# Kernel tuning notes

Measured on AMD Instinct MI355X. Metric: run time of the kernel, lower is better.

## Reference

```python
import jax, jax.numpy as jnp
import numpy as np

EPS = 1e-6

def setup_inputs() -> dict:
    key = jax.random.key(0)
    ks = jax.random.split(key, 8)
    B, C, H, W = 8, 256, 128, 128
    d = C // 8  # scale=8
    return {
        "x": jax.random.normal(ks[0], (B, C, H, W), dtype=jnp.float32),
        "wq": jax.random.normal(ks[1], (d, C), dtype=jnp.float32) * 0.05,
        "bq": jax.random.normal(ks[2], (d,), dtype=jnp.float32) * 0.05,
        "wk": jax.random.normal(ks[3], (d, C), dtype=jnp.float32) * 0.05,
        "bk": jax.random.normal(ks[4], (d,), dtype=jnp.float32) * 0.05,
        "wv": jax.random.normal(ks[5], (C, C), dtype=jnp.float32) * 0.05,
        "bv": jax.random.normal(ks[6], (C,), dtype=jnp.float32) * 0.05,
        "gamma": jax.random.normal(ks[7], (1,), dtype=jnp.float32) * 0.05,
    }

def reference(x, wq, bq, wk, bk, wv, bv, gamma):
    B, C, H, W = x.shape
    N = H * W
    xf = x.reshape(B, C, N)  # flatten spatial
    # 1x1 convs == channel-mixing matmuls
    Q = jax.nn.softplus(jnp.einsum('dc,bcn->bnd', wq, xf) + bq[None, None, :])  # [B,N,d]
    K = jax.nn.softplus(jnp.einsum('dc,bcn->bdn', wk, xf) + bk[None, :, None])  # [B,d,N]
    V = jnp.einsum('ec,bcn->ben', wv, xf) + bv[None, :, None]                    # [B,C,N]
    KV = jnp.einsum('bmn,bcn->bmc', K, V)                # [B,d,C]
    norm = 1.0 / jnp.einsum('bnm,bm->bn', Q, K.sum(-1) + EPS)  # [B,N]
    wv_out = jnp.einsum('bnm,bmc,bn->bcn', Q, KV, norm)  # [B,C,N]
    return x + gamma * wv_out.reshape(B, C, H, W)
```

## Files before the change

kernel.cpp:

```cpp
#include <hip/hip_runtime.h>

#define NB 8
#define NC 256
#define ND 32
#define NN 16384
#define EPSF 1e-6f

__device__ __forceinline__ float softplusf(float v) {
    return fmaxf(v, 0.0f) + log1pf(__expf(-fabsf(v)));
}

__global__ __launch_bounds__(256) void kA(
    const float* __restrict__ x, const float* __restrict__ wk,
    const float* __restrict__ bk, float* __restrict__ part,
    float* __restrict__ kxf, float* __restrict__ ksum, int use_part)
{
    __shared__ __align__(16) float xsT[32 * 258];
    __shared__ __align__(16) float wkM[32 * 260];
    __shared__ __align__(16) float Ks [32 * 36];

    const int t    = threadIdx.x;
    const int b    = blockIdx.x >> 6;
    const int tile = blockIdx.x & 63;
    const int n0   = tile << 8;
    const float* xb = x + (size_t)b * NC * NN;

    #pragma unroll
    for (int i = 0; i < 32; ++i) {
        int f = t + (i << 8);
        wkM[(f >> 8) * 260 + (f & 255)] = wk[f];
    }

    const int jA  = t & 31;
    const int m0A = (t >> 5) << 2;
    const int m0X = (t >> 6) << 3;
    const int eX  = t & 63;

    float bkr[4];
    #pragma unroll
    for (int r = 0; r < 4; ++r) bkr[r] = bk[m0A + r];

    float acc[8][4];
    #pragma unroll
    for (int a = 0; a < 8; ++a)
        #pragma unroll
        for (int kk = 0; kk < 4; ++kk) acc[a][kk] = 0.0f;
    float ksacc[4] = {0.f, 0.f, 0.f, 0.f};

    for (int st = 0; st < 8; ++st) {
        const int n1 = n0 + (st << 5);
        __syncthreads();
        #pragma unroll
        for (int i = 0; i < 32; ++i) {
            int f = t + (i << 8);
            int c = f >> 5, j = f & 31;
            xsT[j * 258 + c] = xb[c * NN + n1 + j];
        }
        __syncthreads();

        float kacc[4] = {0.f, 0.f, 0.f, 0.f};
        #pragma unroll 4
        for (int c = 0; c < 256; c += 4) {
            float2 xa = *(const float2*)&xsT[jA * 258 + c];
            float2 xc = *(const float2*)&xsT[jA * 258 + c + 2];
            #pragma unroll
            for (int r = 0; r < 4; ++r) {
                float4 w = *(const float4*)&wkM[(m0A + r) * 260 + c];
                kacc[r] = fmaf(xa.x, w.x, kacc[r]);
                kacc[r] = fmaf(xa.y, w.y, kacc[r]);
                kacc[r] = fmaf(xc.x, w.z, kacc[r]);
                kacc[r] = fmaf(xc.y, w.w, kacc[r]);
            }
        }
        #pragma unroll
        for (int r = 0; r < 4; ++r) {
            float kv_ = softplusf(kacc[r] + bkr[r]);
            Ks[jA * 36 + m0A + r] = kv_;
            ksacc[r] += kv_;
        }
        __syncthreads();

        #pragma unroll 2
        for (int j = 0; j < 32; ++j) {
            const float* kp = &Ks[j * 36 + m0X];
            float4 ka = *(const float4*)kp;
            float4 kb = *(const float4*)(kp + 4);
            const float km[8] = {ka.x, ka.y, ka.z, ka.w, kb.x, kb.y, kb.z, kb.w};
            float xv[4];
            #pragma unroll
            for (int kk = 0; kk < 4; ++kk) xv[kk] = xsT[j * 258 + eX + (kk << 6)];
            #pragma unroll
            for (int a = 0; a < 8; ++a)
                #pragma unroll
                for (int kk = 0; kk < 4; ++kk)
                    acc[a][kk] = fmaf(km[a], xv[kk], acc[a][kk]);
        }
    }

    #pragma unroll
    for (int r = 0; r < 4; ++r) {
        float v = ksacc[r];
        for (int o = 16; o; o >>= 1) v += __shfl_down(v, o, 32);
        if (jA == 0) atomicAdd(&ksum[b * 32 + m0A + r], v);
    }

    if (use_part) {
        float* dst = part + (size_t)blockIdx.x * 8192;
        #pragma unroll
        for (int a = 0; a < 8; ++a)
            #pragma unroll
            for (int kk = 0; kk < 4; ++kk)
                dst[(m0X + a) * 256 + eX + (kk << 6)] = acc[a][kk];
    } else {
        float* dst = kxf + (size_t)b * 8192;
        #pragma unroll
        for (int a = 0; a < 8; ++a)
            #pragma unroll
            for (int kk = 0; kk < 4; ++kk)
                atomicAdd(&dst[(m0X + a) * 256 + eX + (kk << 6)], acc[a][kk]);
    }
}

__global__ __launch_bounds__(256) void kR(const float* __restrict__ part,
                                          float* __restrict__ kxf)
{
    int idx = blockIdx.x * 256 + threadIdx.x;
    int b = idx >> 13, f = idx & 8191;
    float s = 0.f;
    #pragma unroll 8
    for (int tl = 0; tl < 64; ++tl)
        s += part[(size_t)(b * 64 + tl) * 8192 + f];
    kxf[idx] = s;
}

__global__ __launch_bounds__(256) void kB(
    const float* __restrict__ kxf, const float* __restrict__ ksum,
    const float* __restrict__ wv, const float* __restrict__ bv,
    float* __restrict__ kv)
{
    __shared__ float wvT[256 * 33];
    __shared__ float kxs[32 * 257];

    const int t  = threadIdx.x;
    const int b  = blockIdx.x >> 3;
    const int c0 = (blockIdx.x & 7) << 5;

    #pragma unroll
    for (int i = 0; i < 32; ++i) {
        int f = t + (i << 8);
        int r = f >> 8, e = f & 255;
        wvT[e * 33 + r]  = wv[(size_t)(c0 + r) * 256 + e];
        kxs[r * 257 + e] = kxf[b * 8192 + f];
    }
    __syncthreads();

    const int cl = t & 31, mq = t >> 5;
    float a0 = 0.f, a1 = 0.f, a2 = 0.f, a3 = 0.f;
    for (int e = 0; e < 256; ++e) {
        float wvv = wvT[e * 33 + cl];
        a0 = fmaf(kxs[(mq     ) * 257 + e], wvv, a0);
        a1 = fmaf(kxs[(mq +  8) * 257 + e], wvv, a1);
        a2 = fmaf(kxs[(mq + 16) * 257 + e], wvv, a2);
        a3 = fmaf(kxs[(mq + 24) * 257 + e], wvv, a3);
    }
    const int c = c0 + cl;
    const float bvc = bv[c];
    const float* ks = ksum + b * 32;
    float* kvb = kv + (size_t)b * 8192;
    kvb[(mq     ) * 256 + c] = a0 + bvc * ks[mq     ];
    kvb[(mq +  8) * 256 + c] = a1 + bvc * ks[mq +  8];
    kvb[(mq + 16) * 256 + c] = a2 + bvc * ks[mq + 16];
    kvb[(mq + 24) * 256 + c] = a3 + bvc * ks[mq + 24];
}

__global__ __launch_bounds__(512) void kC(
    const float* __restrict__ x, const float* __restrict__ wq,
    const float* __restrict__ bq, const float* __restrict__ kv,
    const float* __restrict__ ksum, const float* __restrict__ gamma,
    float* __restrict__ out)
{
    __shared__ __align__(16) float xs [256 * 64];
    __shared__ __align__(16) float wqM[32 * 260];
    __shared__ __align__(16) float Qs [32 * 68];
    __shared__ __align__(16) float KVs[32 * 256];
    __shared__ float ksE[32];

    const int t    = threadIdx.x;
    const int b    = blockIdx.x >> 6;
    const int tile = blockIdx.x & 63;
    const int n0   = tile << 8;
    const float* xb = x + (size_t)b * NC * NN;
    const float g = gamma[0];

    #pragma unroll
    for (int i = 0; i < 16; ++i) {
        int f = t + (i << 9);
        wqM[(f >> 8) * 260 + (f & 255)] = wq[f];
        KVs[f] = kv[(size_t)b * 8192 + f];
    }
    if (t < 32) ksE[t] = ksum[b * 32 + t] + EPSF;

    const int jsQ = t & 15;
    const int mQ  = t >> 4;
    const float bqm = bq[mQ];
    const int jO  = t & 63;
    const int c0O = (t >> 6) << 5;

    for (int st = 0; st < 4; ++st) {
        const int n1 = n0 + (st << 6);
        __syncthreads();
        #pragma unroll
        for (int i = 0; i < 32; ++i) {
            int f = t + (i << 9);
            int c = f >> 6, j = f & 63;
            xs[f] = xb[c * NN + n1 + j];
        }
        __syncthreads();

        float qa[4] = {0.f, 0.f, 0.f, 0.f};
        #pragma unroll 4
        for (int c = 0; c < 256; c += 4) {
            float4 w  = *(const float4*)&wqM[mQ * 260 + c];
            float4 x0 = *(const float4*)&xs[(c + 0) * 64 + (jsQ << 2)];
            float4 x1 = *(const float4*)&xs[(c + 1) * 64 + (jsQ << 2)];
            float4 x2 = *(const float4*)&xs[(c + 2) * 64 + (jsQ << 2)];
            float4 x3 = *(const float4*)&xs[(c + 3) * 64 + (jsQ << 2)];
            qa[0] = fmaf(w.x, x0.x, qa[0]); qa[0] = fmaf(w.y, x1.x, qa[0]);
            qa[0] = fmaf(w.z, x2.x, qa[0]); qa[0] = fmaf(w.w, x3.x, qa[0]);
            qa[1] = fmaf(w.x, x0.y, qa[1]); qa[1] = fmaf(w.y, x1.y, qa[1]);
            qa[1] = fmaf(w.z, x2.y, qa[1]); qa[1] = fmaf(w.w, x3.y, qa[1]);
            qa[2] = fmaf(w.x, x0.z, qa[2]); qa[2] = fmaf(w.y, x1.z, qa[2]);
            qa[2] = fmaf(w.z, x2.z, qa[2]); qa[2] = fmaf(w.w, x3.z, qa[2]);
            qa[3] = fmaf(w.x, x0.w, qa[3]); qa[3] = fmaf(w.y, x1.w, qa[3]);
            qa[3] = fmaf(w.z, x2.w, qa[3]); qa[3] = fmaf(w.w, x3.w, qa[3]);
        }
        #pragma unroll
        for (int r = 0; r < 4; ++r)
            Qs[mQ * 68 + (jsQ << 2) + r] = softplusf(qa[r] + bqm);
        __syncthreads();

        float q[32];
        #pragma unroll
        for (int m = 0; m < 32; ++m) q[m] = Qs[m * 68 + jO];
        float den = 0.f;
        #pragma unroll
        for (int m = 0; m < 32; ++m) den = fmaf(q[m], ksE[m], den);
        const float nrm = g / den;

        #pragma unroll
        for (int cc = 0; cc < 8; ++cc) {
            const int c = c0O + (cc << 2);
            float s0 = 0.f, s1 = 0.f, s2 = 0.f, s3 = 0.f;
            #pragma unroll
            for (int m = 0; m < 32; ++m) {
                float4 kvv = *(const float4*)&KVs[m * 256 + c];
                s0 = fmaf(q[m], kvv.x, s0);
                s1 = fmaf(q[m], kvv.y, s1);
                s2 = fmaf(q[m], kvv.z, s2);
                s3 = fmaf(q[m], kvv.w, s3);
            }
            size_t base = (size_t)b * NC * NN + (size_t)c * NN + n1 + jO;
            out[base         ] = xs[(c + 0) * 64 + jO] + nrm * s0;
            out[base +     NN] = xs[(c + 1) * 64 + jO] + nrm * s1;
            out[base + 2 * NN] = xs[(c + 2) * 64 + jO] + nrm * s2;
            out[base + 3 * NN] = xs[(c + 3) * 64 + jO] + nrm * s3;
        }
    }
}

extern "C" void kernel_launch(void* const* d_in, const int* in_sizes, int n_in,
                              void* d_out, int out_size, void* d_ws, size_t ws_size,
                              hipStream_t stream)
{
    (void)in_sizes; (void)n_in; (void)out_size;
    const float* x     = (const float*)d_in[0];
    const float* wq    = (const float*)d_in[1];
    const float* bq    = (const float*)d_in[2];
    const float* wk    = (const float*)d_in[3];
    const float* bk    = (const float*)d_in[4];
    const float* wv    = (const float*)d_in[5];
    const float* bv    = (const float*)d_in[6];
    const float* gamma = (const float*)d_in[7];
    float* out = (float*)d_out;

    char* ws = (char*)d_ws;
    float* kxf  = (float*)(ws);
    float* ksum = (float*)(ws + 262144);
    float* kv   = (float*)(ws + 263168);
    float* part = (float*)(ws + 525312);
    const size_t need_part = 525312ull + 512ull * 8192ull * 4ull;
    const int use_part = (ws_size >= need_part) ? 1 : 0;

    hipMemsetAsync(ksum, 0, 1024, stream);
    if (!use_part) hipMemsetAsync(kxf, 0, 262144, stream);

    kA<<<dim3(512), dim3(256), 0, stream>>>(x, wk, bk, part, kxf, ksum, use_part);
    if (use_part) kR<<<dim3(256), dim3(256), 0, stream>>>(part, kxf);
    kB<<<dim3(64), dim3(256), 0, stream>>>(kxf, ksum, wv, bv, kv);
    kC<<<dim3(512), dim3(512), 0, stream>>>(x, wq, bq, kv, ksum, gamma, out);
}
```

Before: 435.1 us.

## Use bf16 MFMA for K/Q projections, KX accumulation and output in kA/kC

Rewrites the channel-mixing matmuls in kA and kC to use bf16 16x16x32 MFMA instructions, with fp32 inputs converted to bf16 in registers and LDS. kC is retiled into 1024 blocks of 256 threads, and the residual x is re-read from global memory instead of staged fp32 in LDS. The aim is to replace scalar FMA loops with matrix-core throughput and to cut LDS footprint so more blocks fit per CU. The cost is bf16 rounding in Q, K, x and KV, which may reduce accuracy, plus extra global reads of x.

```diff
diff --git a/kernel.cpp b/kernel.cpp
--- a/kernel.cpp
+++ b/kernel.cpp
@@ -1,4 +1,5 @@
 #include <hip/hip_runtime.h>
+#include <hip/hip_bf16.h>
 
 #define NB 8
 #define NC 256
@@ -6,8 +7,19 @@
 #define NN 16384
 #define EPSF 1e-6f
 
+typedef __attribute__((ext_vector_type(8))) short short8;
+typedef __attribute__((ext_vector_type(4))) float float4v;
+
 __device__ __forceinline__ float softplusf(float v) {
     return fmaxf(v, 0.0f) + log1pf(__expf(-fabsf(v)));
+}
+
+__device__ __forceinline__ unsigned short f2bf(float f) {
+    __hip_bfloat16 h = __float2bfloat16(f);
+    return *reinterpret_cast<unsigned short*>(&h);
+}
+__device__ __forceinline__ unsigned int pk2bf(float lo, float hi) {
+    return (unsigned int)f2bf(lo) | ((unsigned int)f2bf(hi) << 16);
 }
 
 __global__ __launch_bounds__(256) void kA(
@@ -15,109 +27,116 @@
     const float* __restrict__ bk, float* __restrict__ part,
     float* __restrict__ kxf, float* __restrict__ ksum, int use_part)
 {
-    __shared__ __align__(16) float xsT[32 * 258];
-    __shared__ __align__(16) float wkM[32 * 260];
-    __shared__ __align__(16) float Ks [32 * 36];
-
-    const int t    = threadIdx.x;
-    const int b    = blockIdx.x >> 6;
-    const int tile = blockIdx.x & 63;
-    const int n0   = tile << 8;
+    __shared__ __align__(16) unsigned char smem[35840];
+    unsigned short* xsT = (unsigned short*)smem;
+    float*          KXs = (float*)smem;
+    unsigned short* Klt = (unsigned short*)(smem + 33280);
+
+    const int t  = threadIdx.x;
+    const int b  = blockIdx.x >> 6;
+    const int n0 = (blockIdx.x & 63) << 8;
     const float* xb = x + (size_t)b * NC * NN;
 
-    #pragma unroll
-    for (int i = 0; i < 32; ++i) {
-        int f = t + (i << 8);
-        wkM[(f >> 8) * 260 + (f & 255)] = wk[f];
-    }
-
-    const int jA  = t & 31;
-    const int m0A = (t >> 5) << 2;
-    const int m0X = (t >> 6) << 3;
-    const int eX  = t & 63;
-
+    const int w = t >> 6, l = t & 63, q = l >> 4, ln = l & 15;
+    const int mt = w & 1, ct = w >> 1;
+
+    short8 wkf[8];
+    #pragma unroll
+    for (int ks = 0; ks < 8; ++ks) {
+        const float* wp = wk + (16 * mt + ln) * 256 + 32 * ks + 8 * q;
+        float4 a = *(const float4*)wp;
+        float4 c = *(const float4*)(wp + 4);
+        short8 f;
+        f[0] = (short)f2bf(a.x); f[1] = (short)f2bf(a.y);
+        f[2] = (short)f2bf(a.z); f[3] = (short)f2bf(a.w);
+        f[4] = (short)f2bf(c.x); f[5] = (short)f2bf(c.y);
+        f[6] = (short)f2bf(c.z); f[7] = (short)f2bf(c.w);
+        wkf[ks] = f;
+    }
     float bkr[4];
     #pragma unroll
-    for (int r = 0; r < 4; ++r) bkr[r] = bk[m0A + r];
-
-    float acc[8][4];
-    #pragma unroll
-    for (int a = 0; a < 8; ++a)
-        #pragma unroll
-        for (int kk = 0; kk < 4; ++kk) acc[a][kk] = 0.0f;
-    float ksacc[4] = {0.f, 0.f, 0.f, 0.f};
-
-    for (int st = 0; st < 8; ++st) {
-        const int n1 = n0 + (st << 5);
-        __syncthreads();
-        #pragma unroll
-        for (int i = 0; i < 32; ++i) {
-            int f = t + (i << 8);
-            int c = f >> 5, j = f & 31;
-            xsT[j * 258 + c] = xb[c * NN + n1 + j];
-        }
-        __syncthreads();
-
-        float kacc[4] = {0.f, 0.f, 0.f, 0.f};
-        #pragma unroll 4
-        for (int c = 0; c < 256; c += 4) {
-            float2 xa = *(const float2*)&xsT[jA * 258 + c];
-            float2 xc = *(const float2*)&xsT[jA * 258 + c + 2];
-            #pragma unroll
-            for (int r = 0; r < 4; ++r) {
-                float4 w = *(const float4*)&wkM[(m0A + r) * 260 + c];
-                kacc[r] = fmaf(xa.x, w.x, kacc[r]);
-                kacc[r] = fmaf(xa.y, w.y, kacc[r]);
-                kacc[r] = fmaf(xc.x, w.z, kacc[r]);
-                kacc[r] = fmaf(xc.y, w.w, kacc[r]);
-            }
+    for (int r = 0; r < 4; ++r) bkr[r] = bk[16 * mt + 4 * q + r];
+
+    float ksumacc[4] = {0.f, 0.f, 0.f, 0.f};
+    float4v kxacc[4][2];
+    #pragma unroll
+    for (int i = 0; i < 4; ++i)
+        #pragma unroll
+        for (int m2 = 0; m2 < 2; ++m2) kxacc[i][m2] = (float4v){0.f, 0.f, 0.f, 0.f};
+    const float4v zf = {0.f, 0.f, 0.f, 0.f};
+
+    for (int ch = 0; ch < 8; ++ch) {
+        const int nc = n0 + (ch << 5);
+        __syncthreads();
+        #pragma unroll
+        for (int i = 0; i < 16; ++i) {
+            int p = t + (i << 8);
+            int n_ = p & 31, cp = p >> 5;
+            float v0 = xb[(size_t)(2 * cp) * NN + nc + n_];
+            float v1 = xb[(size_t)(2 * cp + 1) * NN + nc + n_];
+            *(unsigned int*)&xsT[n_ * 264 + 2 * cp] = pk2bf(v0, v1);
+        }
+        __syncthreads();
+
+        float4v kacc = zf;
+        const int ncol = 16 * ct + ln;
+        #pragma unroll
+        for (int ks = 0; ks < 8; ++ks) {
+            short8 bfr = *(const short8*)&xsT[ncol * 264 + 32 * ks + 8 * q];
+            kacc = __builtin_amdgcn_mfma_f32_16x16x32_bf16(wkf[ks], bfr, kacc, 0, 0, 0);
         }
         #pragma unroll
         for (int r = 0; r < 4; ++r) {
             float kv_ = softplusf(kacc[r] + bkr[r]);
-            Ks[jA * 36 + m0A + r] = kv_;
-            ksacc[r] += kv_;
-        }
-        __syncthreads();
-
-        #pragma unroll 2
-        for (int j = 0; j < 32; ++j) {
-            const float* kp = &Ks[j * 36 + m0X];
-            float4 ka = *(const float4*)kp;
-            float4 kb = *(const float4*)(kp + 4);
-            const float km[8] = {ka.x, ka.y, ka.z, ka.w, kb.x, kb.y, kb.z, kb.w};
-            float xv[4];
+            ksumacc[r] += kv_;
+            Klt[(16 * mt + 4 * q + r) * 40 + ncol] = f2bf(kv_);
+        }
+        __syncthreads();
+
+        #pragma unroll
+        for (int i = 0; i < 4; ++i) {
+            const int e = 16 * (4 * w + i) + ln;
+            const float* xp = xb + (size_t)e * NN + nc + 8 * q;
+            float4 xa = *(const float4*)xp;
+            float4 xc = *(const float4*)(xp + 4);
+            short8 af;
+            af[0] = (short)f2bf(xa.x); af[1] = (short)f2bf(xa.y);
+            af[2] = (short)f2bf(xa.z); af[3] = (short)f2bf(xa.w);
+            af[4] = (short)f2bf(xc.x); af[5] = (short)f2bf(xc.y);
+            af[6] = (short)f2bf(xc.z); af[7] = (short)f2bf(xc.w);
             #pragma unroll
-            for (int kk = 0; kk < 4; ++kk) xv[kk] = xsT[j * 258 + eX + (kk << 6)];
+            for (int m2 = 0; m2 < 2; ++m2) {
+                short8 bfr = *(const short8*)&Klt[(16 * m2 + ln) * 40 + 8 * q];
+                kxacc[i][m2] = __builtin_amdgcn_mfma_f32_16x16x32_bf16(af, bfr, kxacc[i][m2], 0, 0, 0);
+            }
+        }
+    }
+
+    #pragma unroll
+    for (int r = 0; r < 4; ++r) {
+        float v = ksumacc[r];
+        v += __shfl_xor(v, 1); v += __shfl_xor(v, 2);
+        v += __shfl_xor(v, 4); v += __shfl_xor(v, 8);
+        if (ln == 0) atomicAdd(&ksum[b * 32 + 16 * mt + 4 * q + r], v);
+    }
+
+    __syncthreads();
+    #pragma unroll
+    for (int i = 0; i < 4; ++i)
+        #pragma unroll
+        for (int m2 = 0; m2 < 2; ++m2)
             #pragma unroll
-            for (int a = 0; a < 8; ++a)
-                #pragma unroll
-                for (int kk = 0; kk < 4; ++kk)
-                    acc[a][kk] = fmaf(km[a], xv[kk], acc[a][kk]);
-        }
-    }
-
-    #pragma unroll
-    for (int r = 0; r < 4; ++r) {
-        float v = ksacc[r];
-        for (int o = 16; o; o >>= 1) v += __shfl_down(v, o, 32);
-        if (jA == 0) atomicAdd(&ksum[b * 32 + m0A + r], v);
-    }
-
+            for (int r = 0; r < 4; ++r)
+                KXs[(16 * m2 + ln) * 260 + 16 * (4 * w + i) + 4 * q + r] = kxacc[i][m2][r];
+    __syncthreads();
     if (use_part) {
         float* dst = part + (size_t)blockIdx.x * 8192;
         #pragma unroll
-        for (int a = 0; a < 8; ++a)
-            #pragma unroll
-            for (int kk = 0; kk < 4; ++kk)
-                dst[(m0X + a) * 256 + eX + (kk << 6)] = acc[a][kk];
+        for (int i = 0; i < 32; ++i) dst[i * 256 + t] = KXs[i * 260 + t];
     } else {
         float* dst = kxf + (size_t)b * 8192;
         #pragma unroll
-        for (int a = 0; a < 8; ++a)
-            #pragma unroll
-            for (int kk = 0; kk < 4; ++kk)
-                atomicAdd(&dst[(m0X + a) * 256 + eX + (kk << 6)], acc[a][kk]);
+        for (int i = 0; i < 32; ++i) atomicAdd(&dst[i * 256 + t], KXs[i * 260 + t]);
     }
 }
 
@@ -173,97 +192,108 @@
     kvb[(mq + 24) * 256 + c] = a3 + bvc * ks[mq + 24];
 }
 
-__global__ __launch_bounds__(512) void kC(
+__global__ __launch_bounds__(256) void kC(
     const float* __restrict__ x, const float* __restrict__ wq,
     const float* __restrict__ bq, const float* __restrict__ kv,
     const float* __restrict__ ksum, const float* __restrict__ gamma,
     float* __restrict__ out)
 {
-    __shared__ __align__(16) float xs [256 * 64];
-    __shared__ __align__(16) float wqM[32 * 260];
-    __shared__ __align__(16) float Qs [32 * 68];
-    __shared__ __align__(16) float KVs[32 * 256];
-    __shared__ float ksE[32];
-
-    const int t    = threadIdx.x;
-    const int b    = blockIdx.x >> 6;
-    const int tile = blockIdx.x & 63;
-    const int n0   = tile << 8;
+    __shared__ __align__(16) unsigned short xsT[32 * 264];
+    __shared__ __align__(16) unsigned short Qs [32 * 40];
+    __shared__ float denp[2 * 32];
+
+    const int t  = threadIdx.x;
+    const int b  = blockIdx.x >> 7;
+    const int n0 = (blockIdx.x & 127) << 5 << 2;
     const float* xb = x + (size_t)b * NC * NN;
+    float* ob = out + (size_t)b * NC * NN;
     const float g = gamma[0];
 
-    #pragma unroll
-    for (int i = 0; i < 16; ++i) {
-        int f = t + (i << 9);
-        wqM[(f >> 8) * 260 + (f & 255)] = wq[f];
-        KVs[f] = kv[(size_t)b * 8192 + f];
-    }
-    if (t < 32) ksE[t] = ksum[b * 32 + t] + EPSF;
-
-    const int jsQ = t & 15;
-    const int mQ  = t >> 4;
-    const float bqm = bq[mQ];
-    const int jO  = t & 63;
-    const int c0O = (t >> 6) << 5;
-
-    for (int st = 0; st < 4; ++st) {
-        const int n1 = n0 + (st << 6);
-        __syncthreads();
-        #pragma unroll
-        for (int i = 0; i < 32; ++i) {
-            int f = t + (i << 9);
-            int c = f >> 6, j = f & 63;
-            xs[f] = xb[c * NN + n1 + j];
-        }
-        __syncthreads();
-
-        float qa[4] = {0.f, 0.f, 0.f, 0.f};
-        #pragma unroll 4
-        for (int c = 0; c < 256; c += 4) {
-            float4 w  = *(const float4*)&wqM[mQ * 260 + c];
-            float4 x0 = *(const float4*)&xs[(c + 0) * 64 + (jsQ << 2)];
-            float4 x1 = *(const float4*)&xs[(c + 1) * 64 + (jsQ << 2)];
-            float4 x2 = *(const float4*)&xs[(c + 2) * 64 + (jsQ << 2)];
-            float4 x3 = *(const float4*)&xs[(c + 3) * 64 + (jsQ << 2)];
-            qa[0] = fmaf(w.x, x0.x, qa[0]); qa[0] = fmaf(w.y, x1.x, qa[0]);
-            qa[0] = fmaf(w.z, x2.x, qa[0]); qa[0] = fmaf(w.w, x3.x, qa[0]);
-            qa[1] = fmaf(w.x, x0.y, qa[1]); qa[1] = fmaf(w.y, x1.y, qa[1]);
-            qa[1] = fmaf(w.z, x2.y, qa[1]); qa[1] = fmaf(w.w, x3.y, qa[1]);
-            qa[2] = fmaf(w.x, x0.z, qa[2]); qa[2] = fmaf(w.y, x1.z, qa[2]);
-            qa[2] = fmaf(w.z, x2.z, qa[2]); qa[2] = fmaf(w.w, x3.z, qa[2]);
-            qa[3] = fmaf(w.x, x0.w, qa[3]); qa[3] = fmaf(w.y, x1.w, qa[3]);
-            qa[3] = fmaf(w.z, x2.w, qa[3]); qa[3] = fmaf(w.w, x3.w, qa[3]);
-        }
-        #pragma unroll
-        for (int r = 0; r < 4; ++r)
-            Qs[mQ * 68 + (jsQ << 2) + r] = softplusf(qa[r] + bqm);
-        __syncthreads();
-
-        float q[32];
-        #pragma unroll
-        for (int m = 0; m < 32; ++m) q[m] = Qs[m * 68 + jO];
-        float den = 0.f;
-        #pragma unroll
-        for (int m = 0; m < 32; ++m) den = fmaf(q[m], ksE[m], den);
-        const float nrm = g / den;
-
-        #pragma unroll
-        for (int cc = 0; cc < 8; ++cc) {
-            const int c = c0O + (cc << 2);
-            float s0 = 0.f, s1 = 0.f, s2 = 0.f, s3 = 0.f;
+    const int w = t >> 6, l = t & 63, q = l >> 4, ln = l & 15;
+    const int mt = w & 1, ct = w >> 1;
+
+    short8 wqf[8];
+    #pragma unroll
+    for (int ks = 0; ks < 8; ++ks) {
+        const float* wp = wq + (16 * mt + ln) * 256 + 32 * ks + 8 * q;
+        float4 a = *(const float4*)wp;
+        float4 c = *(const float4*)(wp + 4);
+        short8 f;
+        f[0] = (short)f2bf(a.x); f[1] = (short)f2bf(a.y);
+        f[2] = (short)f2bf(a.z); f[3] = (short)f2bf(a.w);
+        f[4] = (short)f2bf(c.x); f[5] = (short)f2bf(c.y);
+        f[6] = (short)f2bf(c.z); f[7] = (short)f2bf(c.w);
+        wqf[ks] = f;
+    }
+    float bqr[4], ksEr[4];
+    #pragma unroll
+    for (int r = 0; r < 4; ++r) {
+        bqr[r]  = bq[16 * mt + 4 * q + r];
+        ksEr[r] = ksum[b * 32 + 16 * mt + 4 * q + r] + EPSF;
+    }
+    short8 kvf[4];
+    #pragma unroll
+    for (int cc = 0; cc < 4; ++cc) {
+        const float* kp = kv + (size_t)b * 8192 + (8 * q) * 256 + 16 * (4 * w + cc) + ln;
+        short8 f;
+        #pragma unroll
+        for (int j = 0; j < 8; ++j) f[j] = (short)f2bf(kp[j * 256]);
+        kvf[cc] = f;
+    }
+    const float4v zf = {0.f, 0.f, 0.f, 0.f};
+
+    for (int ch = 0; ch < 4; ++ch) {
+        const int nc = n0 + (ch << 5);
+        __syncthreads();
+        #pragma unroll
+        for (int i = 0; i < 16; ++i) {
+            int p = t + (i << 8);
+            int n_ = p & 31, cp = p >> 5;
+            float v0 = xb[(size_t)(2 * cp) * NN + nc + n_];
+            float v1 = xb[(size_t)(2 * cp + 1) * NN + nc + n_];
+            *(unsigned int*)&xsT[n_ * 264 + 2 * cp] = pk2bf(v0, v1);
+        }
+        __syncthreads();
+
+        float4v qacc = zf;
+        const int ncol = 16 * ct + ln;
+        #pragma unroll
+        for (int ks = 0; ks < 8; ++ks) {
+            short8 bfr = *(const short8*)&xsT[ncol * 264 + 32 * ks + 8 * q];
+            qacc = __builtin_amdgcn_mfma_f32_16x16x32_bf16(wqf[ks], bfr, qacc, 0, 0, 0);
+        }
+        float dpart = 0.f;
+        unsigned short qpk[4];
+        #pragma unroll
+        for (int r = 0; r < 4; ++r) {
+            float qv = softplusf(qacc[r] + bqr[r]);
+            dpart += qv * ksEr[r];
+            qpk[r] = f2bf(qv);
+        }
+        *(unsigned int*)&Qs[ncol * 40 + 16 * mt + 4 * q]     = (unsigned int)qpk[0] | ((unsigned int)qpk[1] << 16);
+        *(unsigned int*)&Qs[ncol * 40 + 16 * mt + 4 * q + 2] = (unsigned int)qpk[2] | ((unsigned int)qpk[3] << 16);
+        dpart += __shfl_xor(dpart, 16);
+        dpart += __shfl_xor(dpart, 32);
+        if (l < 16) denp[mt * 32 + 16 * ct + l] = dpart;
+        __syncthreads();
+
+        #pragma unroll
+        for (int ctn = 0; ctn < 2; ++ctn) {
+            const int ncol2 = 16 * ctn + ln;
+            const float den = denp[ncol2] + denp[32 + ncol2];
+            const float nrm = g / den;
+            short8 bqf = *(const short8*)&Qs[ncol2 * 40 + 8 * q];
+            const int ngl = nc + ncol2;
             #pragma unroll
-            for (int m = 0; m < 32; ++m) {
-                float4 kvv = *(const float4*)&KVs[m * 256 + c];
-                s0 = fmaf(q[m], kvv.x, s0);
-                s1 = fmaf(q[m], kvv.y, s1);
-                s2 = fmaf(q[m], kvv.z, s2);
-                s3 = fmaf(q[m], kvv.w, s3);
+            for (int cc = 0; cc < 4; ++cc) {
+                float4v p = __builtin_amdgcn_mfma_f32_16x16x32_bf16(kvf[cc], bqf, zf, 0, 0, 0);
+                #pragma unroll
+                for (int r = 0; r < 4; ++r) {
+                    const int c = 16 * (4 * w + cc) + 4 * q + r;
+                    size_t addr = (size_t)c * NN + ngl;
+                    ob[addr] = xb[addr] + nrm * p[r];
+                }
             }
-            size_t base = (size_t)b * NC * NN + (size_t)c * NN + n1 + jO;
-            out[base         ] = xs[(c + 0) * 64 + jO] + nrm * s0;
-            out[base +     NN] = xs[(c + 1) * 64 + jO] + nrm * s1;
-            out[base + 2 * NN] = xs[(c + 2) * 64 + jO] + nrm * s2;
-            out[base + 3 * NN] = xs[(c + 3) * 64 + jO] + nrm * s3;
         }
     }
 }
@@ -297,5 +327,5 @@
     kA<<<dim3(512), dim3(256), 0, stream>>>(x, wk, bk, part, kxf, ksum, use_part);
     if (use_part) kR<<<dim3(256), dim3(256), 0, stream>>>(part, kxf);
     kB<<<dim3(64), dim3(256), 0, stream>>>(kxf, ksum, wv, bv, kv);
-    kC<<<dim3(512), dim3(512), 0, stream>>>(x, wq, bq, kv, ksum, gamma, out);
-}
+    kC<<<dim3(1024), dim3(256), 0, stream>>>(x, wq, bq, kv, ksum, gamma, out);
+}
```

Result: slower. 450.4 us (+3.5%).
